# Kernel optimization log

Measured on AMD Instinct MI355X. Metric: run time of the kernel, lower is better.

The kernel has to match this reference:

```python
import jax, jax.numpy as jnp
import numpy as np

OPS_SIZE = (40, 40, 40)
ALPHA = 0.005
BETA = 0.01


def _disp_from_landmarks(coords, values):
    # coords, values: (N,3). Returns (3, W0, H0, D0) coarse displacement field.
    D0, H0, W0 = OPS_SIZE
    axes = [jnp.linspace(-1.0, 1.0, s) for s in OPS_SIZE]
    grid = jnp.stack(jnp.meshgrid(*axes, indexing='ij'), -1).reshape(-1, 3)  # (G,3)
    # squared distance ||g - c||^2 via expansion (avoids (N,G,3) repeat tensor)
    d2 = (jnp.sum(grid * grid, -1)[:, None]
          + jnp.sum(coords * coords, -1)[None, :]
          - 2.0 * grid @ coords.T)  # (G,N)
    w = jnp.exp(-d2 / ALPHA)
    w = (BETA + 1.0) * w / (jnp.sum(w, axis=1, keepdims=True) + BETA)
    disp = (w @ values).reshape(D0, H0, W0, 3)
    return jnp.transpose(disp, (3, 2, 1, 0))  # torch permute(3,2,1,0)


def _interp_axis(x, axis, out_s):
    # 1D linear resize along `axis`, matching F.interpolate align_corners=False
    in_s = x.shape[axis]
    c = jnp.maximum((jnp.arange(out_s, dtype=jnp.float32) + 0.5) * (in_s / out_s) - 0.5, 0.0)
    i0 = jnp.minimum(jnp.floor(c).astype(jnp.int32), in_s - 1)
    i1 = jnp.minimum(i0 + 1, in_s - 1)
    t = (c - i0.astype(jnp.float32)).astype(x.dtype)
    shp = [1] * x.ndim
    shp[axis] = out_s
    t = t.reshape(shp)
    return jnp.take(x, i0, axis=axis) * (1 - t) + jnp.take(x, i1, axis=axis) * t


def _resize_trilinear(x, out_size):
    # x: (C, d, h, w) -> (C, D, H, W); trilinear resize is separable
    for ax, s in zip((1, 2, 3), out_size):
        x = _interp_axis(x, ax, s)
    return x


def _grid_sample_3d(vol, grid):
    # vol: (B,C,D,H,W), grid: (B,Do,Ho,Wo,3), grid[...,0]=x indexes W.
    # mode='bilinear' (trilinear), padding_mode='zeros', align_corners=False
    B, C, D, H, W = vol.shape
    x = ((grid[..., 0] + 1.0) * W - 1.0) / 2.0
    y = ((grid[..., 1] + 1.0) * H - 1.0) / 2.0
    z = ((grid[..., 2] + 1.0) * D - 1.0) / 2.0

    def per_batch(v, x, y, z):
        x0 = jnp.floor(x); y0 = jnp.floor(y); z0 = jnp.floor(z)
        fx = x - x0; fy = y - y0; fz = z - z0
        x0i = x0.astype(jnp.int32); y0i = y0.astype(jnp.int32); z0i = z0.astype(jnp.int32)
        acc = jnp.zeros((C,) + x.shape, v.dtype)
        for dz in (0, 1):
            wz = fz if dz else 1.0 - fz
            zi = z0i + dz
            for dy in (0, 1):
                wy = fy if dy else 1.0 - fy
                yi = y0i + dy
                for dx in (0, 1):
                    wx = fx if dx else 1.0 - fx
                    xi = x0i + dx
                    m = ((zi >= 0) & (zi < D) & (yi >= 0) & (yi < H) & (xi >= 0) & (xi < W)).astype(v.dtype)
                    zc = jnp.clip(zi, 0, D - 1); yc = jnp.clip(yi, 0, H - 1); xc = jnp.clip(xi, 0, W - 1)
                    acc = acc + v[:, zc, yc, xc] * ((wz * wy * wx * m)[None])
        return acc

    return jax.vmap(per_batch)(vol, x, y, z)


def reference(orgin_mask, control_points_coords, control_points_offsets):
    B, C, D, H, W = orgin_mask.shape
    coords = control_points_coords + control_points_offsets  # (B,N,3)
    vals = -control_points_offsets                            # (B,N,3)
    disp = jax.vmap(_disp_from_landmarks)(coords, vals)       # (B,3,W0,H0,D0)
    flow = jax.vmap(lambda d: _resize_trilinear(d, (D, H, W)))(disp)  # (B,3,D,H,W)
    axes = [jnp.linspace(-1.0, 1.0, s) for s in (D, H, W)]
    base = jnp.stack(jnp.meshgrid(*axes, indexing='ij'), 0)   # (3,D,H,W)
    base = jnp.transpose(base, (0, 3, 2, 1))                  # torch permute(0,1,4,3,2); needs D==H==W
    warped = base[None] + flow                                # (B,3,D,H,W)
    warped = jnp.transpose(warped, (0, 2, 3, 4, 1))           # (B,D,H,W,3)
    return _grid_sample_3d(orgin_mask, warped)


def setup_inputs() -> dict:
    key = jax.random.key(0)
    k1, k2, k3 = jax.random.split(key, 3)
    orgin_mask = jax.random.uniform(k1, (2, 1, 128, 128, 128), dtype=jnp.float32)
    control_points_coords = jax.random.uniform(k2, (2, 1024, 3), dtype=jnp.float32, minval=-1.0, maxval=1.0)
    control_points_offsets = jax.random.normal(k3, (2, 1024, 3), dtype=jnp.float32) * 0.05
    return {"orgin_mask": orgin_mask,
            "control_points_coords": control_points_coords,
            "control_points_offsets": control_points_offsets}
```

## Files before the change

kernel.cpp:

```cpp
#include <hip/hip_runtime.h>
#include <math.h>

#define NLM   1024
#define NB    2
#define OPS   40
#define DIM   128
#define OPS3  (OPS*OPS*OPS)
#define DIM3  (DIM*DIM*DIM)

#define TILE   8
#define NTILE  (OPS/TILE)
#define CPT    4
#define MARGIN 0.30f

#define K2f  (-288.5390081777927f)
#define M2f  ( 577.0780163555854f)


__device__ __forceinline__ float fexp2(float x) {
#if __has_builtin(__builtin_amdgcn_exp2f)
    return __builtin_amdgcn_exp2f(x);
#else
    return exp2f(x);
#endif
}

__global__ __launch_bounds__(128)
void coarse_kernel(const float* __restrict__ coords, const float* __restrict__ offs,
                   float4* __restrict__ C) {
    __shared__ float4 sA[NLM];
    __shared__ float4 sV[NLM];
    __shared__ int sCnt;

    const int t = threadIdx.x;
    const int b = blockIdx.y;
    const int tile = blockIdx.x;
    const int tp = tile / (NTILE*NTILE);
    const int tq = (tile / NTILE) % NTILE;
    const int tr = tile % NTILE;

    const float step = 2.f / (OPS - 1);
    const float bx0 = -1.f + step * (tr*TILE)          - MARGIN;
    const float bx1 = -1.f + step * (tr*TILE + TILE-1) + MARGIN;
    const float by0 = -1.f + step * (tq*TILE)          - MARGIN;
    const float by1 = -1.f + step * (tq*TILE + TILE-1) + MARGIN;
    const float bz0 = -1.f + step * (tp*TILE)          - MARGIN;
    const float bz1 = -1.f + step * (tp*TILE + TILE-1) + MARGIN;

    if (t == 0) sCnt = 0;
    __syncthreads();

    for (int n = t; n < NLM; n += 128) {
        const float* cp = coords + (b*NLM + n)*3;
        const float* op = offs   + (b*NLM + n)*3;
        float ox = op[0], oy = op[1], oz = op[2];
        float cx = cp[0] + ox, cy = cp[1] + oy, cz = cp[2] + oz;
        if (cx >= bx0 && cx <= bx1 && cy >= by0 && cy <= by1 &&
            cz >= bz0 && cz <= bz1) {
            int idx = atomicAdd(&sCnt, 1);
            sA[idx] = make_float4(cx, cy, cz, K2f*(cx*cx + cy*cy + cz*cz));
            sV[idx] = make_float4(-ox, -oy, -oz, 0.f);
        }
    }
    __syncthreads();
    const int cnt = sCnt;

    float gx[CPT], gy[CPT], gz[CPT], h[CPT];
    #pragma unroll
    for (int c = 0; c < CPT; ++c) {
        int local = c*128 + t;
        int lp = local >> 6, lq = (local >> 3) & 7, lr = local & 7;
        gx[c] = -1.f + step * (tr*TILE + lr);
        gy[c] = -1.f + step * (tq*TILE + lq);
        gz[c] = -1.f + step * (tp*TILE + lp);
        h[c]  = K2f * (gx[c]*gx[c] + gy[c]*gy[c] + gz[c]*gz[c]);
    }

    float4 acc[CPT];
    #pragma unroll
    for (int c = 0; c < CPT; ++c) acc[c] = make_float4(0.f, 0.f, 0.f, 0.f);

    for (int n = 0; n < cnt; ++n) {
        float4 a = sA[n];
        float4 v = sV[n];
        #pragma unroll
        for (int c = 0; c < CPT; ++c) {
            float u   = fmaf(gx[c], a.x, fmaf(gy[c], a.y, gz[c]*a.z));
            float arg = fmaf(M2f, u, h[c] + a.w);
            float e   = fexp2(arg);
            acc[c].x += e;
            acc[c].y  = fmaf(e, v.x, acc[c].y);
            acc[c].z  = fmaf(e, v.y, acc[c].z);
            acc[c].w  = fmaf(e, v.z, acc[c].w);
        }
    }

    #pragma unroll
    for (int c = 0; c < CPT; ++c) {
        int local = c*128 + t;
        int lp = local >> 6, lq = (local >> 3) & 7, lr = local & 7;
        int p = tp*TILE + lp, q = tq*TILE + lq, r = tr*TILE + lr;
        float inv = 1.01f / (acc[c].x + 0.01f);
        C[b*OPS3 + (p*OPS + q)*OPS + r] =
            make_float4(acc[c].y*inv, acc[c].z*inv, acc[c].w*inv, 0.f);
    }
}

__device__ __forceinline__ void axis_interp(int t, int& a0, int& a1, float& w) {
    float c = fmaxf(0.3125f * (float)t - 0.34375f, 0.f);
    float f = floorf(c);
    a0 = (int)f;
    a1 = min(a0 + 1, OPS - 1);
    w = c - f;
}

__device__ __forceinline__ float4 lerp4(float4 a, float4 b, float t) {
    return make_float4(a.x + t*(b.x - a.x),
                       a.y + t*(b.y - a.y),
                       a.z + t*(b.z - a.z),
                       0.f);
}

__global__ __launch_bounds__(64)
void warp_kernel(const float* __restrict__ mask, const float4* __restrict__ C,
                 float* __restrict__ out) {
    __shared__ float4 sF[OPS];

    const int blk  = blockIdx.x;
    const int line = ((blk & 7) << 12) + (blk >> 3);
    const int j = line & (DIM-1);
    const int i = (line >> 7) & (DIM-1);
    const int b = line >> 14;

    int i0,i1,j0,j1; float ti,tj;
    axis_interp(i, i0, i1, ti);
    axis_interp(j, j0, j1, tj);

    const float4* Cb = C + b*OPS3;
    const int t = threadIdx.x;
    if (t < OPS) {
        float4 c00 = Cb[(i0*OPS + j0)*OPS + t];
        float4 c01 = Cb[(i0*OPS + j1)*OPS + t];
        float4 c10 = Cb[(i1*OPS + j0)*OPS + t];
        float4 c11 = Cb[(i1*OPS + j1)*OPS + t];
        sF[t] = lerp4(lerp4(c00, c01, tj), lerp4(c10, c11, tj), ti);
    }
    __syncthreads();

    const float* M = mask + b * DIM3;
    const float s127 = 2.f / (DIM - 1);
    const float yb = -1.f + s127 * (float)j;
    const float zb = -1.f + s127 * (float)i;

    float res[2];
    #pragma unroll
    for (int c = 0; c < 2; ++c) {
        const int k = t + 64*c;
        int k0,k1; float tk;
        axis_interp(k, k0, k1, tk);
        float4 fl = lerp4(sF[k0], sF[k1], tk);

        float x = -1.f + s127 * (float)k + fl.x;
        float y = yb + fl.y;
        float z = zb + fl.z;

        float px = ((x + 1.f) * (float)DIM - 1.f) * 0.5f;
        float py = ((y + 1.f) * (float)DIM - 1.f) * 0.5f;
        float pz = ((z + 1.f) * (float)DIM - 1.f) * 0.5f;

        float xf = floorf(px), yf = floorf(py), zf = floorf(pz);
        int   x0 = (int)xf,    y0 = (int)yf,    z0 = (int)zf;
        float ax = px - xf,    ay = py - yf,    az = pz - zf;

        float acc = 0.f;
        #pragma unroll
        for (int dz = 0; dz < 2; dz++) {
            int zi = z0 + dz;
            bool zin = (unsigned)zi < (unsigned)DIM;
            int zc = min(max(zi, 0), DIM-1);
            float wz = dz ? az : 1.f - az;
            #pragma unroll
            for (int dy = 0; dy < 2; dy++) {
                int yi = y0 + dy;
                bool yin = (unsigned)yi < (unsigned)DIM;
                int yc = min(max(yi, 0), DIM-1);
                float wy = dy ? ay : 1.f - ay;
                #pragma unroll
                for (int dx = 0; dx < 2; dx++) {
                    int xi = x0 + dx;
                    bool xin = (unsigned)xi < (unsigned)DIM;
                    int xc = min(max(xi, 0), DIM-1);
                    float wx = dx ? ax : 1.f - ax;
                    float v = (zin && yin && xin) ? M[(zc*DIM + yc)*DIM + xc] : 0.f;
                    acc = fmaf(v, wz*wy*wx, acc);
                }
            }
        }
        res[c] = acc;
    }
    out[(line << 7) + t]      = res[0];
    out[(line << 7) + t + 64] = res[1];
}

extern "C" void kernel_launch(void* const* d_in, const int* in_sizes, int n_in,
                              void* d_out, int out_size, void* d_ws, size_t ws_size,
                              hipStream_t stream) {
    const float* mask   = (const float*)d_in[0];
    const float* coords = (const float*)d_in[1];
    const float* offs   = (const float*)d_in[2];
    float* out = (float*)d_out;

    float4* coarse = (float4*)d_ws;

    dim3 g1(NTILE*NTILE*NTILE, NB);
    coarse_kernel<<<g1, 128, 0, stream>>>(coords, offs, coarse);

    warp_kernel<<<NB*DIM*DIM, 64, 0, stream>>>(mask, coarse, out);
}
```

Measured before the change: 122.2 us.

## Add interior fast path for trilinear gather and pack four lines per block

Result: faster. 111.0 us (-9.2%).

```diff
diff --git a/kernel.cpp b/kernel.cpp
--- a/kernel.cpp
+++ b/kernel.cpp
@@ -121,13 +121,67 @@
                        0.f);
 }
 
-__global__ __launch_bounds__(64)
+struct Samp { int rb; float ax, ay, az; bool fast; int x0, y0, z0; };
+
+__device__ __forceinline__ Samp make_samp(float px, float py, float pz) {
+    Samp s;
+    float xf = floorf(px), yf = floorf(py), zf = floorf(pz);
+    s.x0 = (int)xf; s.y0 = (int)yf; s.z0 = (int)zf;
+    s.ax = px - xf; s.ay = py - yf; s.az = pz - zf;
+    s.fast = ((unsigned)s.x0 < 127u) & ((unsigned)s.y0 < 127u) & ((unsigned)s.z0 < 127u);
+    s.rb = (s.z0*DIM + s.y0)*DIM + s.x0;
+    return s;
+}
+
+__device__ __forceinline__ float slow_gather(const float* __restrict__ M, const Samp& s) {
+    float acc = 0.f;
+    #pragma unroll
+    for (int dz = 0; dz < 2; dz++) {
+        int zi = s.z0 + dz;
+        bool zin = (unsigned)zi < (unsigned)DIM;
+        int zc = min(max(zi, 0), DIM-1);
+        float wz = dz ? s.az : 1.f - s.az;
+        #pragma unroll
+        for (int dy = 0; dy < 2; dy++) {
+            int yi = s.y0 + dy;
+            bool yin = (unsigned)yi < (unsigned)DIM;
+            int yc = min(max(yi, 0), DIM-1);
+            float wy = dy ? s.ay : 1.f - s.ay;
+            #pragma unroll
+            for (int dx = 0; dx < 2; dx++) {
+                int xi = s.x0 + dx;
+                bool xin = (unsigned)xi < (unsigned)DIM;
+                int xc = min(max(xi, 0), DIM-1);
+                float wx = dx ? s.ax : 1.f - s.ax;
+                float v = (zin && yin && xin) ? M[(zc*DIM + yc)*DIM + xc] : 0.f;
+                acc = fmaf(v, wz*wy*wx, acc);
+            }
+        }
+    }
+    return acc;
+}
+
+__device__ __forceinline__ float tri8(float v000, float v001, float v010, float v011,
+                                      float v100, float v101, float v110, float v111,
+                                      float ax, float ay, float az) {
+    float c00 = fmaf(ax, v001 - v000, v000);
+    float c01 = fmaf(ax, v011 - v010, v010);
+    float c10 = fmaf(ax, v101 - v100, v100);
+    float c11 = fmaf(ax, v111 - v110, v110);
+    float c0  = fmaf(ay, c01 - c00, c00);
+    float c1  = fmaf(ay, c11 - c10, c10);
+    return fmaf(az, c1 - c0, c0);
+}
+
+__global__ __launch_bounds__(256)
 void warp_kernel(const float* __restrict__ mask, const float4* __restrict__ C,
                  float* __restrict__ out) {
-    __shared__ float4 sF[OPS];
-
-    const int blk  = blockIdx.x;
-    const int line = ((blk & 7) << 12) + (blk >> 3);
+    __shared__ float4 sF[4][OPS];
+
+    const int g = blockIdx.x;
+    const int w = threadIdx.x >> 6;
+    const int lane = threadIdx.x & 63;
+    const int line = ((g & 7) << 12) + ((g >> 3) << 2) + w;
     const int j = line & (DIM-1);
     const int i = (line >> 7) & (DIM-1);
     const int b = line >> 14;
@@ -137,69 +191,56 @@
     axis_interp(j, j0, j1, tj);
 
     const float4* Cb = C + b*OPS3;
-    const int t = threadIdx.x;
-    if (t < OPS) {
-        float4 c00 = Cb[(i0*OPS + j0)*OPS + t];
-        float4 c01 = Cb[(i0*OPS + j1)*OPS + t];
-        float4 c10 = Cb[(i1*OPS + j0)*OPS + t];
-        float4 c11 = Cb[(i1*OPS + j1)*OPS + t];
-        sF[t] = lerp4(lerp4(c00, c01, tj), lerp4(c10, c11, tj), ti);
-    }
-    __syncthreads();
+    if (lane < OPS) {
+        float4 c00 = Cb[(i0*OPS + j0)*OPS + lane];
+        float4 c01 = Cb[(i0*OPS + j1)*OPS + lane];
+        float4 c10 = Cb[(i1*OPS + j0)*OPS + lane];
+        float4 c11 = Cb[(i1*OPS + j1)*OPS + lane];
+        sF[w][lane] = lerp4(lerp4(c00, c01, tj), lerp4(c10, c11, tj), ti);
+    }
 
     const float* M = mask + b * DIM3;
     const float s127 = 2.f / (DIM - 1);
     const float yb = -1.f + s127 * (float)j;
     const float zb = -1.f + s127 * (float)i;
 
-    float res[2];
+    Samp sp[2];
     #pragma unroll
     for (int c = 0; c < 2; ++c) {
-        const int k = t + 64*c;
+        const int k = lane + 64*c;
         int k0,k1; float tk;
         axis_interp(k, k0, k1, tk);
-        float4 fl = lerp4(sF[k0], sF[k1], tk);
-
+        float4 fl = lerp4(sF[w][k0], sF[w][k1], tk);
         float x = -1.f + s127 * (float)k + fl.x;
         float y = yb + fl.y;
         float z = zb + fl.z;
-
-        float px = ((x + 1.f) * (float)DIM - 1.f) * 0.5f;
-        float py = ((y + 1.f) * (float)DIM - 1.f) * 0.5f;
-        float pz = ((z + 1.f) * (float)DIM - 1.f) * 0.5f;
-
-        float xf = floorf(px), yf = floorf(py), zf = floorf(pz);
-        int   x0 = (int)xf,    y0 = (int)yf,    z0 = (int)zf;
-        float ax = px - xf,    ay = py - yf,    az = pz - zf;
-
-        float acc = 0.f;
-        #pragma unroll
-        for (int dz = 0; dz < 2; dz++) {
-            int zi = z0 + dz;
-            bool zin = (unsigned)zi < (unsigned)DIM;
-            int zc = min(max(zi, 0), DIM-1);
-            float wz = dz ? az : 1.f - az;
-            #pragma unroll
-            for (int dy = 0; dy < 2; dy++) {
-                int yi = y0 + dy;
-                bool yin = (unsigned)yi < (unsigned)DIM;
-                int yc = min(max(yi, 0), DIM-1);
-                float wy = dy ? ay : 1.f - ay;
-                #pragma unroll
-                for (int dx = 0; dx < 2; dx++) {
-                    int xi = x0 + dx;
-                    bool xin = (unsigned)xi < (unsigned)DIM;
-                    int xc = min(max(xi, 0), DIM-1);
-                    float wx = dx ? ax : 1.f - ax;
-                    float v = (zin && yin && xin) ? M[(zc*DIM + yc)*DIM + xc] : 0.f;
-                    acc = fmaf(v, wz*wy*wx, acc);
-                }
-            }
-        }
-        res[c] = acc;
-    }
-    out[(line << 7) + t]      = res[0];
-    out[(line << 7) + t + 64] = res[1];
+        sp[c] = make_samp(((x + 1.f) * (float)DIM - 1.f) * 0.5f,
+                          ((y + 1.f) * (float)DIM - 1.f) * 0.5f,
+                          ((z + 1.f) * (float)DIM - 1.f) * 0.5f);
+    }
+
+    float res[2];
+    if (sp[0].fast && sp[1].fast) {
+        const int rb0 = sp[0].rb, rb1 = sp[1].rb;
+        float a000 = M[rb0], a001 = M[rb0+1];
+        float a010 = M[rb0+DIM], a011 = M[rb0+DIM+1];
+        float a100 = M[rb0+DIM*DIM], a101 = M[rb0+DIM*DIM+1];
+        float a110 = M[rb0+DIM*DIM+DIM], a111 = M[rb0+DIM*DIM+DIM+1];
+        float b000 = M[rb1], b001 = M[rb1+1];
+        float b010 = M[rb1+DIM], b011 = M[rb1+DIM+1];
+        float b100 = M[rb1+DIM*DIM], b101 = M[rb1+DIM*DIM+1];
+        float b110 = M[rb1+DIM*DIM+DIM], b111 = M[rb1+DIM*DIM+DIM+1];
+        res[0] = tri8(a000,a001,a010,a011,a100,a101,a110,a111,
+                      sp[0].ax, sp[0].ay, sp[0].az);
+        res[1] = tri8(b000,b001,b010,b011,b100,b101,b110,b111,
+                      sp[1].ax, sp[1].ay, sp[1].az);
+    } else {
+        res[0] = slow_gather(M, sp[0]);
+        res[1] = slow_gather(M, sp[1]);
+    }
+
+    out[(line << 7) + lane]      = res[0];
+    out[(line << 7) + lane + 64] = res[1];
 }
 
 extern "C" void kernel_launch(void* const* d_in, const int* in_sizes, int n_in,
@@ -215,5 +256,5 @@
     dim3 g1(NTILE*NTILE*NTILE, NB);
     coarse_kernel<<<g1, 128, 0, stream>>>(coords, offs, coarse);
 
-    warp_kernel<<<NB*DIM*DIM, 64, 0, stream>>>(mask, coarse, out);
-}
+    warp_kernel<<<NB*DIM*DIM/4, 256, 0, stream>>>(mask, coarse, out);
+}
```

## Shrink coarse tiles and batch trilinear gathers over multiple lines per block

Applied to the files above, without the earlier changes.

Result: faster. 113.9 us (-6.8%).

```diff
diff --git a/kernel.cpp b/kernel.cpp
--- a/kernel.cpp
+++ b/kernel.cpp
@@ -8,9 +8,12 @@
 #define OPS3  (OPS*OPS*OPS)
 #define DIM3  (DIM*DIM*DIM)
 
-#define TILE   8
-#define NTILE  (OPS/TILE)
-#define CPT    4
+#define P_T 4
+#define Q_T 4
+#define R_T 8
+#define NP  (OPS/P_T)
+#define NQ  (OPS/Q_T)
+#define NR  (OPS/R_T)
 #define MARGIN 0.30f
 
 #define K2f  (-288.5390081777927f)
@@ -35,17 +38,17 @@
     const int t = threadIdx.x;
     const int b = blockIdx.y;
     const int tile = blockIdx.x;
-    const int tp = tile / (NTILE*NTILE);
-    const int tq = (tile / NTILE) % NTILE;
-    const int tr = tile % NTILE;
+    const int tp = tile / (NQ*NR);
+    const int tq = (tile / NR) % NQ;
+    const int tr = tile % NR;
 
     const float step = 2.f / (OPS - 1);
-    const float bx0 = -1.f + step * (tr*TILE)          - MARGIN;
-    const float bx1 = -1.f + step * (tr*TILE + TILE-1) + MARGIN;
-    const float by0 = -1.f + step * (tq*TILE)          - MARGIN;
-    const float by1 = -1.f + step * (tq*TILE + TILE-1) + MARGIN;
-    const float bz0 = -1.f + step * (tp*TILE)          - MARGIN;
-    const float bz1 = -1.f + step * (tp*TILE + TILE-1) + MARGIN;
+    const float bx0 = -1.f + step * (tr*R_T)          - MARGIN;
+    const float bx1 = -1.f + step * (tr*R_T + R_T-1)  + MARGIN;
+    const float by0 = -1.f + step * (tq*Q_T)          - MARGIN;
+    const float by1 = -1.f + step * (tq*Q_T + Q_T-1)  + MARGIN;
+    const float bz0 = -1.f + step * (tp*P_T)          - MARGIN;
+    const float bz1 = -1.f + step * (tp*P_T + P_T-1)  + MARGIN;
 
     if (t == 0) sCnt = 0;
     __syncthreads();
@@ -65,45 +68,30 @@
     __syncthreads();
     const int cnt = sCnt;
 
-    float gx[CPT], gy[CPT], gz[CPT], h[CPT];
-    #pragma unroll
-    for (int c = 0; c < CPT; ++c) {
-        int local = c*128 + t;
-        int lp = local >> 6, lq = (local >> 3) & 7, lr = local & 7;
-        gx[c] = -1.f + step * (tr*TILE + lr);
-        gy[c] = -1.f + step * (tq*TILE + lq);
-        gz[c] = -1.f + step * (tp*TILE + lp);
-        h[c]  = K2f * (gx[c]*gx[c] + gy[c]*gy[c] + gz[c]*gz[c]);
-    }
-
-    float4 acc[CPT];
-    #pragma unroll
-    for (int c = 0; c < CPT; ++c) acc[c] = make_float4(0.f, 0.f, 0.f, 0.f);
-
+    const int lp = t >> 5;
+    const int lq = (t >> 3) & 3;
+    const int lr = t & 7;
+    const float gx = -1.f + step * (tr*R_T + lr);
+    const float gy = -1.f + step * (tq*Q_T + lq);
+    const float gz = -1.f + step * (tp*P_T + lp);
+    const float h  = K2f * (gx*gx + gy*gy + gz*gz);
+
+    float aS = 0.f, aX = 0.f, aY = 0.f, aZ = 0.f;
     for (int n = 0; n < cnt; ++n) {
         float4 a = sA[n];
         float4 v = sV[n];
-        #pragma unroll
-        for (int c = 0; c < CPT; ++c) {
-            float u   = fmaf(gx[c], a.x, fmaf(gy[c], a.y, gz[c]*a.z));
-            float arg = fmaf(M2f, u, h[c] + a.w);
-            float e   = fexp2(arg);
-            acc[c].x += e;
-            acc[c].y  = fmaf(e, v.x, acc[c].y);
-            acc[c].z  = fmaf(e, v.y, acc[c].z);
-            acc[c].w  = fmaf(e, v.z, acc[c].w);
-        }
-    }
-
-    #pragma unroll
-    for (int c = 0; c < CPT; ++c) {
-        int local = c*128 + t;
-        int lp = local >> 6, lq = (local >> 3) & 7, lr = local & 7;
-        int p = tp*TILE + lp, q = tq*TILE + lq, r = tr*TILE + lr;
-        float inv = 1.01f / (acc[c].x + 0.01f);
-        C[b*OPS3 + (p*OPS + q)*OPS + r] =
-            make_float4(acc[c].y*inv, acc[c].z*inv, acc[c].w*inv, 0.f);
-    }
+        float u   = fmaf(gx, a.x, fmaf(gy, a.y, gz*a.z));
+        float arg = fmaf(M2f, u, h + a.w);
+        float e   = fexp2(arg);
+        aS += e;
+        aX = fmaf(e, v.x, aX);
+        aY = fmaf(e, v.y, aY);
+        aZ = fmaf(e, v.z, aZ);
+    }
+
+    const int p = tp*P_T + lp, q = tq*Q_T + lq, r = tr*R_T + lr;
+    const float inv = 1.01f / (aS + 0.01f);
+    C[b*OPS3 + (p*OPS + q)*OPS + r] = make_float4(aX*inv, aY*inv, aZ*inv, 0.f);
 }
 
 __device__ __forceinline__ void axis_interp(int t, int& a0, int& a1, float& w) {
@@ -121,85 +109,121 @@
                        0.f);
 }
 
-__global__ __launch_bounds__(64)
+__global__ __launch_bounds__(256)
 void warp_kernel(const float* __restrict__ mask, const float4* __restrict__ C,
                  float* __restrict__ out) {
-    __shared__ float4 sF[OPS];
-
-    const int blk  = blockIdx.x;
-    const int line = ((blk & 7) << 12) + (blk >> 3);
-    const int j = line & (DIM-1);
-    const int i = (line >> 7) & (DIM-1);
-    const int b = line >> 14;
-
-    int i0,i1,j0,j1; float ti,tj;
-    axis_interp(i, i0, i1, ti);
-    axis_interp(j, j0, j1, tj);
-
-    const float4* Cb = C + b*OPS3;
-    const int t = threadIdx.x;
-    if (t < OPS) {
-        float4 c00 = Cb[(i0*OPS + j0)*OPS + t];
-        float4 c01 = Cb[(i0*OPS + j1)*OPS + t];
-        float4 c10 = Cb[(i1*OPS + j0)*OPS + t];
-        float4 c11 = Cb[(i1*OPS + j1)*OPS + t];
-        sF[t] = lerp4(lerp4(c00, c01, tj), lerp4(c10, c11, tj), ti);
-    }
-    __syncthreads();
-
-    const float* M = mask + b * DIM3;
+    __shared__ float4 sF[8][OPS];
+
+    const int g = blockIdx.x;
+    const int w = threadIdx.x >> 6;
+    const int lane = threadIdx.x & 63;
+    const int line0 = ((g & 7) << 12) + ((g >> 3) << 3) + (w << 1);
+
     const float s127 = 2.f / (DIM - 1);
-    const float yb = -1.f + s127 * (float)j;
-    const float zb = -1.f + s127 * (float)i;
-
-    float res[2];
-    #pragma unroll
-    for (int c = 0; c < 2; ++c) {
-        const int k = t + 64*c;
-        int k0,k1; float tk;
-        axis_interp(k, k0, k1, tk);
-        float4 fl = lerp4(sF[k0], sF[k1], tk);
-
-        float x = -1.f + s127 * (float)k + fl.x;
-        float y = yb + fl.y;
-        float z = zb + fl.z;
-
-        float px = ((x + 1.f) * (float)DIM - 1.f) * 0.5f;
-        float py = ((y + 1.f) * (float)DIM - 1.f) * 0.5f;
-        float pz = ((z + 1.f) * (float)DIM - 1.f) * 0.5f;
-
-        float xf = floorf(px), yf = floorf(py), zf = floorf(pz);
-        int   x0 = (int)xf,    y0 = (int)yf,    z0 = (int)zf;
-        float ax = px - xf,    ay = py - yf,    az = pz - zf;
-
-        float acc = 0.f;
+
+    #pragma unroll
+    for (int e = 0; e < 2; ++e) {
+        const int line = line0 + e;
+        const int j = line & (DIM-1);
+        const int i = (line >> 7) & (DIM-1);
+        const int b = line >> 14;
+        int i0,i1,j0,j1; float ti,tj;
+        axis_interp(i, i0, i1, ti);
+        axis_interp(j, j0, j1, tj);
+        const float4* Cb = C + b*OPS3;
+        if (lane < OPS) {
+            float4 c00 = Cb[(i0*OPS + j0)*OPS + lane];
+            float4 c01 = Cb[(i0*OPS + j1)*OPS + lane];
+            float4 c10 = Cb[(i1*OPS + j0)*OPS + lane];
+            float4 c11 = Cb[(i1*OPS + j1)*OPS + lane];
+            sF[(w<<1)+e][lane] = lerp4(lerp4(c00, c01, tj), lerp4(c10, c11, tj), ti);
+        }
+    }
+
+    int   off[4][6];
+    float wt[4][6];
+    int   oidx[4];
+    const float* Mv[4];
+    #pragma unroll
+    for (int e = 0; e < 2; ++e) {
+        const int line = line0 + e;
+        const int j = line & (DIM-1);
+        const int i = (line >> 7) & (DIM-1);
+        const int b = line >> 14;
+        const float yb = -1.f + s127 * (float)j;
+        const float zb = -1.f + s127 * (float)i;
+        const float* M = mask + b * DIM3;
         #pragma unroll
-        for (int dz = 0; dz < 2; dz++) {
-            int zi = z0 + dz;
-            bool zin = (unsigned)zi < (unsigned)DIM;
-            int zc = min(max(zi, 0), DIM-1);
-            float wz = dz ? az : 1.f - az;
-            #pragma unroll
-            for (int dy = 0; dy < 2; dy++) {
-                int yi = y0 + dy;
-                bool yin = (unsigned)yi < (unsigned)DIM;
-                int yc = min(max(yi, 0), DIM-1);
-                float wy = dy ? ay : 1.f - ay;
-                #pragma unroll
-                for (int dx = 0; dx < 2; dx++) {
-                    int xi = x0 + dx;
-                    bool xin = (unsigned)xi < (unsigned)DIM;
-                    int xc = min(max(xi, 0), DIM-1);
-                    float wx = dx ? ax : 1.f - ax;
-                    float v = (zin && yin && xin) ? M[(zc*DIM + yc)*DIM + xc] : 0.f;
-                    acc = fmaf(v, wz*wy*wx, acc);
-                }
-            }
+        for (int c = 0; c < 2; ++c) {
+            const int vi = e*2 + c;
+            const int k = lane + (c << 6);
+            int k0,k1; float tk;
+            axis_interp(k, k0, k1, tk);
+            float4 fl = lerp4(sF[(w<<1)+e][k0], sF[(w<<1)+e][k1], tk);
+
+            float x = -1.f + s127 * (float)k + fl.x;
+            float y = yb + fl.y;
+            float z = zb + fl.z;
+            float px = ((x + 1.f) * (float)DIM - 1.f) * 0.5f;
+            float py = ((y + 1.f) * (float)DIM - 1.f) * 0.5f;
+            float pz = ((z + 1.f) * (float)DIM - 1.f) * 0.5f;
+
+            float xf = floorf(px), yf = floorf(py), zf = floorf(pz);
+            float ax = px - xf,    ay = py - yf,    az = pz - zf;
+            int x0 = (int)xf, y0 = (int)yf, z0 = (int)zf;
+
+            wt[vi][0] = ((unsigned)x0     < 128u) ? (1.f - ax) : 0.f;
+            wt[vi][1] = ((unsigned)(x0+1) < 128u) ? ax         : 0.f;
+            wt[vi][2] = ((unsigned)y0     < 128u) ? (1.f - ay) : 0.f;
+            wt[vi][3] = ((unsigned)(y0+1) < 128u) ? ay         : 0.f;
+            wt[vi][4] = ((unsigned)z0     < 128u) ? (1.f - az) : 0.f;
+            wt[vi][5] = ((unsigned)(z0+1) < 128u) ? az         : 0.f;
+
+            off[vi][0] = (x0 & 127);
+            off[vi][1] = ((x0+1) & 127);
+            off[vi][2] = (y0 & 127) << 7;
+            off[vi][3] = ((y0+1) & 127) << 7;
+            off[vi][4] = (z0 & 127) << 14;
+            off[vi][5] = ((z0+1) & 127) << 14;
+            Mv[vi]   = M;
+            oidx[vi] = (line << 7) + k;
         }
-        res[c] = acc;
-    }
-    out[(line << 7) + t]      = res[0];
-    out[(line << 7) + t + 64] = res[1];
+    }
+
+    float tv[4][8];
+    #pragma unroll
+    for (int vi = 0; vi < 4; ++vi) {
+        const float* M = Mv[vi];
+        const int xa = off[vi][0], xb = off[vi][1];
+        const int ya = off[vi][2], yc = off[vi][3];
+        const int za = off[vi][4], zc = off[vi][5];
+        tv[vi][0] = M[za + ya + xa];
+        tv[vi][1] = M[za + ya + xb];
+        tv[vi][2] = M[za + yc + xa];
+        tv[vi][3] = M[za + yc + xb];
+        tv[vi][4] = M[zc + ya + xa];
+        tv[vi][5] = M[zc + ya + xb];
+        tv[vi][6] = M[zc + yc + xa];
+        tv[vi][7] = M[zc + yc + xb];
+    }
+
+    #pragma unroll
+    for (int vi = 0; vi < 4; ++vi) {
+        float wx0 = wt[vi][0], wx1 = wt[vi][1];
+        float wy0 = wt[vi][2], wy1 = wt[vi][3];
+        float wz0 = wt[vi][4], wz1 = wt[vi][5];
+        float w00 = wz0*wy0, w01 = wz0*wy1, w10 = wz1*wy0, w11 = wz1*wy1;
+        float r;
+        r = tv[vi][0] * (w00*wx0);
+        r = fmaf(tv[vi][1], w00*wx1, r);
+        r = fmaf(tv[vi][2], w01*wx0, r);
+        r = fmaf(tv[vi][3], w01*wx1, r);
+        r = fmaf(tv[vi][4], w10*wx0, r);
+        r = fmaf(tv[vi][5], w10*wx1, r);
+        r = fmaf(tv[vi][6], w11*wx0, r);
+        r = fmaf(tv[vi][7], w11*wx1, r);
+        out[oidx[vi]] = r;
+    }
 }
 
 extern "C" void kernel_launch(void* const* d_in, const int* in_sizes, int n_in,
@@ -212,8 +236,8 @@
 
     float4* coarse = (float4*)d_ws;
 
-    dim3 g1(NTILE*NTILE*NTILE, NB);
+    dim3 g1(NP*NQ*NR, NB);
     coarse_kernel<<<g1, 128, 0, stream>>>(coords, offs, coarse);
 
-    warp_kernel<<<NB*DIM*DIM, 64, 0, stream>>>(mask, coarse, out);
-}
+    warp_kernel<<<NB*DIM*DIM/8, 256, 0, stream>>>(mask, coarse, out);
+}
```
